# Kernel tuning notes

Hardware: AMD Instinct MI355X
Metric: run time of the kernel (lower is better)

The kernel has to match this reference:

```python
import jax, jax.numpy as jnp
import numpy as np


def setup_inputs() -> dict:
    key = jax.random.key(0)
    N, C, H, W, D = 4, 128, 48, 48, 48
    x = jax.random.normal(key, (N, C, H, W, D), dtype=jnp.float32)
    return {"x": x}


def reference(x) -> jnp.ndarray:
    # Channel self-attention over flattened spatial dims.
    N, C, H, W, D = x.shape
    q = x.reshape(N, C, -1)                      # [N, C, S]
    # energy[n, i, j] = <channel i, channel j>
    energy = jnp.einsum('ncs,nms->ncm', q, q)    # [N, C, C]
    # max-subtract trick (note: softmax of (max - energy), NOT energy - max)
    energy_new = jnp.max(energy, axis=-1, keepdims=True) - energy
    attention = jax.nn.softmax(energy_new, axis=-1)  # [N, C, C]
    out = jnp.einsum('ncm,nms->ncs', attention, q)   # [N, C, S]
    return out.reshape(N, C, H, W, D)
```

## Files before the change

kernel.cpp:

```cpp
#include <hip/hip_runtime.h>
#include <math.h>


static constexpr int CN = 128;
static constexpr int SN = 110592;
static constexpr int NB = 4;

static constexpr int GB = 64;
static constexpr int GSL = SN / GB;
static constexpr int GCH = GSL / 64;

static constexpr int PB = 432;
static constexpr int PCH = 4;

typedef float  f32x4  __attribute__((ext_vector_type(4)));
typedef short  bf16x8 __attribute__((ext_vector_type(8)));
typedef unsigned short u16x8 __attribute__((ext_vector_type(8)));
typedef unsigned short u16x4 __attribute__((ext_vector_type(4)));

__device__ __forceinline__ unsigned int splitpack(float v) {
    unsigned int u = __float_as_uint(v);
    unsigned int h = (u + 0x7fffu + ((u >> 16) & 1u)) >> 16;
    float lf = v - __uint_as_float(h << 16);
    unsigned int ul = __float_as_uint(lf);
    unsigned int l = (ul + 0x7fffu + ((ul >> 16) & 1u)) >> 16;
    return (l << 16) | (h & 0xffffu);
}
__device__ __forceinline__ unsigned short f2bh(float v) {
    unsigned int u = __float_as_uint(v);
    return (unsigned short)((u + 0x7fffu + ((u >> 16) & 1u)) >> 16);
}

__device__ __forceinline__ bf16x8 ldsfrag(const unsigned short* base, int row, int kbyte, int pitchB) {
    const char* p = reinterpret_cast<const char*>(base) + row * pitchB + (kbyte ^ ((row & 7) << 4));
    return *reinterpret_cast<const bf16x8*>(p);
}
__device__ __forceinline__ f32x4 mm(bf16x8 a, bf16x8 b, f32x4 c) {
    return __builtin_amdgcn_mfma_f32_16x16x32_bf16(a, b, c, 0, 0, 0);
}

template <bool ATOMIC>
__global__ __launch_bounds__(512, 2) void gram_mfma(const float* __restrict__ x,
                                                    float* __restrict__ dst) {
    __shared__ __align__(16) unsigned short lh[2][CN * 64];
    __shared__ __align__(16) unsigned short ll[2][CN * 64];
    const int bx = blockIdx.x, n = blockIdx.y;
    const int tid = threadIdx.x;
    const int lane = tid & 63;
    const int w = tid >> 6;
    const int wr = w >> 2, wc = w & 3;
    const int ra = lane & 15, kg = lane >> 4;

    const int c  = tid >> 2;
    const int ks = (tid & 3) << 4;
    const float* gq = x + (size_t)n * CN * SN + (size_t)c * SN + bx * GSL;

    f32x4 acc[4][2];
#pragma unroll
    for (int a = 0; a < 4; ++a)
#pragma unroll
        for (int b = 0; b < 2; ++b) acc[a][b] = (f32x4){0.f, 0.f, 0.f, 0.f};

    float4 st[4];
    auto load_chunk = [&](int t) {
        const float4* p = reinterpret_cast<const float4*>(gq + t * 64 + ks);
        st[0] = p[0]; st[1] = p[1]; st[2] = p[2]; st[3] = p[3];
    };

    auto stage = [&](int buf) {
        u16x8 ha, hb, la, lb;
        unsigned int p;
#define CV8(hv, lv, i, val) { p = splitpack(val); hv[i] = (unsigned short)(p & 0xffffu); lv[i] = (unsigned short)(p >> 16); }
        CV8(ha, la, 0, st[0].x) CV8(ha, la, 1, st[0].y) CV8(ha, la, 2, st[0].z) CV8(ha, la, 3, st[0].w)
        CV8(ha, la, 4, st[1].x) CV8(ha, la, 5, st[1].y) CV8(ha, la, 6, st[1].z) CV8(ha, la, 7, st[1].w)
        CV8(hb, lb, 0, st[2].x) CV8(hb, lb, 1, st[2].y) CV8(hb, lb, 2, st[2].z) CV8(hb, lb, 3, st[2].w)
        CV8(hb, lb, 4, st[3].x) CV8(hb, lb, 5, st[3].y) CV8(hb, lb, 6, st[3].z) CV8(hb, lb, 7, st[3].w)
#undef CV8
        char* ph = reinterpret_cast<char*>(lh[buf]) + c * 128;
        char* pl = reinterpret_cast<char*>(ll[buf]) + c * 128;
        const int sw = (c & 7) << 4;
        const int k2 = ks * 2;
        *reinterpret_cast<u16x8*>(ph + (k2 ^ sw))        = ha;
        *reinterpret_cast<u16x8*>(ph + ((k2 + 16) ^ sw)) = hb;
        *reinterpret_cast<u16x8*>(pl + (k2 ^ sw))        = la;
        *reinterpret_cast<u16x8*>(pl + ((k2 + 16) ^ sw)) = lb;
    };

    auto compute = [&](int buf) {
        const unsigned short* LH = lh[buf];
        const unsigned short* LL = ll[buf];
#pragma unroll
        for (int kk = 0; kk < 2; ++kk) {
            const int kb = kk * 64 + (kg << 4);
            bf16x8 ah[4], al[4], bh[2], bl[2];
#pragma unroll
            for (int it = 0; it < 4; ++it) {
                const int row = wr * 64 + it * 16 + ra;
                ah[it] = ldsfrag(LH, row, kb, 128);
                al[it] = ldsfrag(LL, row, kb, 128);
            }
#pragma unroll
            for (int jt = 0; jt < 2; ++jt) {
                const int row = wc * 32 + jt * 16 + ra;
                bh[jt] = ldsfrag(LH, row, kb, 128);
                bl[jt] = ldsfrag(LL, row, kb, 128);
            }
#pragma unroll
            for (int it = 0; it < 4; ++it)
#pragma unroll
                for (int jt = 0; jt < 2; ++jt) {
                    acc[it][jt] = mm(ah[it], bh[jt], acc[it][jt]);
                    acc[it][jt] = mm(ah[it], bl[jt], acc[it][jt]);
                    acc[it][jt] = mm(al[it], bh[jt], acc[it][jt]);
                }
        }
    };

    load_chunk(0);
    for (int t = 0; t < GCH; ++t) {
        stage(t & 1);
        if (t < GCH - 1) load_chunk(t + 1);
        __syncthreads();
        compute(t & 1);
    }

    const int q4 = kg << 2;
    if (!ATOMIC) {
        float* P = dst + (size_t)(n * GB + bx) * (CN * CN);
#pragma unroll
        for (int it = 0; it < 4; ++it)
#pragma unroll
            for (int jt = 0; jt < 2; ++jt)
#pragma unroll
                for (int q = 0; q < 4; ++q)
                    P[(wr * 64 + it * 16 + q4 + q) * CN + wc * 32 + jt * 16 + ra] = acc[it][jt][q];
    } else {
        float* E = dst + (size_t)n * CN * CN;
#pragma unroll
        for (int it = 0; it < 4; ++it)
#pragma unroll
            for (int jt = 0; jt < 2; ++jt)
#pragma unroll
                for (int q = 0; q < 4; ++q)
                    atomicAdd(&E[(wr * 64 + it * 16 + q4 + q) * CN + wc * 32 + jt * 16 + ra], acc[it][jt][q]);
    }
}

template <bool REDUCE>
__global__ void finish_kernel(const float* __restrict__ src,
                              unsigned short* __restrict__ att_h) {
    const int i = blockIdx.x, n = blockIdx.y, l = threadIdx.x;
    float e0, e1;
    if (REDUCE) {
        const float* p = src + (size_t)n * GB * (CN * CN) + i * CN;
        e0 = 0.f; e1 = 0.f;
#pragma unroll 8
        for (int k = 0; k < GB; ++k) {
            e0 += p[(size_t)k * (CN * CN) + l];
            e1 += p[(size_t)k * (CN * CN) + l + 64];
        }
    } else {
        const float* E = src + ((size_t)n * CN + i) * CN;
        e0 = E[l]; e1 = E[l + 64];
    }
    float m = fminf(e0, e1);
#pragma unroll
    for (int off = 32; off > 0; off >>= 1) m = fminf(m, __shfl_xor(m, off));
    const float p0 = expf(m - e0);
    const float p1 = expf(m - e1);
    float s = p0 + p1;
#pragma unroll
    for (int off = 32; off > 0; off >>= 1) s += __shfl_xor(s, off);
    const float inv = 1.f / s;
    const size_t o = ((size_t)n * CN + i) * CN;
    att_h[o + l]      = f2bh(p0 * inv);
    att_h[o + l + 64] = f2bh(p1 * inv);
}

__global__ __launch_bounds__(512, 4) void pv_mfma(const float* __restrict__ x,
                                                  const unsigned short* __restrict__ att_h,
                                                  float* __restrict__ out) {
    __shared__ __align__(16) unsigned short qh[2][64 * CN];
    const int bx = blockIdx.x, n = blockIdx.y;
    const int tid = threadIdx.x;
    const int lane = tid & 63;
    const int w = tid >> 6;
    const int ra = lane & 15, kg = lane >> 4;

    bf16x8 a_h[4];
    {
        const size_t rowoff = ((size_t)n * CN + w * 16 + ra) * CN + kg * 8;
        const unsigned short* Ah = att_h + rowoff;
#pragma unroll
        for (int kk = 0; kk < 4; ++kk)
            a_h[kk] = *reinterpret_cast<const bf16x8*>(Ah + kk * 32);
    }

    const int j0 = (tid >> 4) * 4;
    const int s0 = (tid & 15) * 4;
    const float* gx = x + (size_t)n * CN * SN;
    const int sbase = bx * (PCH * 64);

    f32x4 st[4];
    auto load_chunk = [&](int sb) {
#pragma unroll
        for (int r = 0; r < 4; ++r)
            st[r] = *reinterpret_cast<const f32x4*>(gx + (size_t)(j0 + r) * SN + sb + s0);
    };

    auto stage = [&](int buf) {
        char* base = reinterpret_cast<char*>(qh[buf]);
#pragma unroll
        for (int r = 0; r < 4; ++r) {
            u16x4 hv;
            hv[0] = f2bh(st[0][r]);
            hv[1] = f2bh(st[1][r]);
            hv[2] = f2bh(st[2][r]);
            hv[3] = f2bh(st[3][r]);
            const int s = s0 + r;
            const int off = s * 256 + ((j0 * 2) ^ ((s & 7) << 4));
            *reinterpret_cast<u16x4*>(base + off) = hv;
        }
    };

    auto compute = [&](int buf, int sb) {
        const unsigned short* Q = qh[buf];
#pragma unroll
        for (int stile = 0; stile < 4; ++stile) {
            f32x4 acc = (f32x4){0.f, 0.f, 0.f, 0.f};
            const int srow = stile * 16 + ra;
#pragma unroll
            for (int kk = 0; kk < 4; ++kk) {
                const int kb = kk * 64 + (kg << 4);
                bf16x8 bh = ldsfrag(Q, srow, kb, 256);
                acc = mm(a_h[kk], bh, acc);
            }
            float* o = out + ((size_t)n * CN + w * 16 + (kg << 2)) * SN + sb + stile * 16 + ra;
#pragma unroll
            for (int q = 0; q < 4; ++q)
                __builtin_nontemporal_store(acc[q], o + (size_t)q * SN);
        }
    };

    load_chunk(sbase);
    for (int t = 0; t < PCH; ++t) {
        stage(t & 1);
        if (t < PCH - 1) load_chunk(sbase + (t + 1) * 64);
        __syncthreads();
        compute(t & 1, sbase + t * 64);
    }
}

extern "C" void kernel_launch(void* const* d_in, const int* in_sizes, int n_in,
                              void* d_out, int out_size, void* d_ws, size_t ws_size,
                              hipStream_t stream) {
    (void)in_sizes; (void)n_in; (void)out_size;
    const float* x = (const float*)d_in[0];
    float* out = (float*)d_out;

    float* energy = (float*)d_ws;
    unsigned short* att_h = (unsigned short*)(energy + (size_t)NB * CN * CN);
    float* part = (float*)(att_h + (size_t)NB * CN * CN);
    const size_t need =
        (size_t)NB * CN * CN * sizeof(float) +
        (size_t)NB * CN * CN * sizeof(unsigned short) +
        (size_t)NB * GB * CN * CN * sizeof(float);

    if (ws_size >= need) {
        gram_mfma<false><<<dim3(GB, NB), 512, 0, stream>>>(x, part);
        finish_kernel<true><<<dim3(CN, NB), 64, 0, stream>>>(part, att_h);
    } else {
        hipMemsetAsync(energy, 0, (size_t)NB * CN * CN * sizeof(float), stream);
        gram_mfma<true><<<dim3(GB, NB), 512, 0, stream>>>(x, energy);
        finish_kernel<false><<<dim3(CN, NB), 64, 0, stream>>>(energy, att_h);
    }
    pv_mfma<<<dim3(PB, NB), 512, 0, stream>>>(x, att_h, out);
}
```

Before: 138.4 us.

## Emit bf16 copy of input in gram kernel and reuse it in PV

```diff
diff --git a/kernel.cpp b/kernel.cpp
--- a/kernel.cpp
+++ b/kernel.cpp
@@ -39,9 +39,10 @@
     return __builtin_amdgcn_mfma_f32_16x16x32_bf16(a, b, c, 0, 0, 0);
 }
 
-template <bool ATOMIC>
+template <bool ATOMIC, bool WRITEXH>
 __global__ __launch_bounds__(512, 2) void gram_mfma(const float* __restrict__ x,
-                                                    float* __restrict__ dst) {
+                                                    float* __restrict__ dst,
+                                                    unsigned short* __restrict__ xh) {
     __shared__ __align__(16) unsigned short lh[2][CN * 64];
     __shared__ __align__(16) unsigned short ll[2][CN * 64];
     const int bx = blockIdx.x, n = blockIdx.y;
@@ -54,6 +55,8 @@
     const int c  = tid >> 2;
     const int ks = (tid & 3) << 4;
     const float* gq = x + (size_t)n * CN * SN + (size_t)c * SN + bx * GSL;
+    unsigned short* gxh = WRITEXH
+        ? xh + (size_t)n * CN * SN + (size_t)c * SN + bx * GSL : nullptr;
 
     f32x4 acc[4][2];
 #pragma unroll
@@ -67,7 +70,7 @@
         st[0] = p[0]; st[1] = p[1]; st[2] = p[2]; st[3] = p[3];
     };
 
-    auto stage = [&](int buf) {
+    auto stage = [&](int buf, int t) {
         u16x8 ha, hb, la, lb;
         unsigned int p;
 #define CV8(hv, lv, i, val) { p = splitpack(val); hv[i] = (unsigned short)(p & 0xffffu); lv[i] = (unsigned short)(p >> 16); }
@@ -84,6 +87,11 @@
         *reinterpret_cast<u16x8*>(ph + ((k2 + 16) ^ sw)) = hb;
         *reinterpret_cast<u16x8*>(pl + (k2 ^ sw))        = la;
         *reinterpret_cast<u16x8*>(pl + ((k2 + 16) ^ sw)) = lb;
+        if (WRITEXH) {
+            unsigned short* q = gxh + t * 64 + ks;
+            *reinterpret_cast<u16x8*>(q)     = ha;
+            *reinterpret_cast<u16x8*>(q + 8) = hb;
+        }
     };
 
     auto compute = [&](int buf) {
@@ -118,7 +126,7 @@
 
     load_chunk(0);
     for (int t = 0; t < GCH; ++t) {
-        stage(t & 1);
+        stage(t & 1, t);
         if (t < GCH - 1) load_chunk(t + 1);
         __syncthreads();
         compute(t & 1);
@@ -133,7 +141,8 @@
             for (int jt = 0; jt < 2; ++jt)
 #pragma unroll
                 for (int q = 0; q < 4; ++q)
-                    P[(wr * 64 + it * 16 + q4 + q) * CN + wc * 32 + jt * 16 + ra] = acc[it][jt][q];
+                    __builtin_nontemporal_store(acc[it][jt][q],
+                        &P[(wr * 64 + it * 16 + q4 + q) * CN + wc * 32 + jt * 16 + ra]);
     } else {
         float* E = dst + (size_t)n * CN * CN;
 #pragma unroll
@@ -156,8 +165,8 @@
         e0 = 0.f; e1 = 0.f;
 #pragma unroll 8
         for (int k = 0; k < GB; ++k) {
-            e0 += p[(size_t)k * (CN * CN) + l];
-            e1 += p[(size_t)k * (CN * CN) + l + 64];
+            e0 += __builtin_nontemporal_load(&p[(size_t)k * (CN * CN) + l]);
+            e1 += __builtin_nontemporal_load(&p[(size_t)k * (CN * CN) + l + 64]);
         }
     } else {
         const float* E = src + ((size_t)n * CN + i) * CN;
@@ -177,7 +186,8 @@
     att_h[o + l + 64] = f2bh(p1 * inv);
 }
 
-__global__ __launch_bounds__(512, 4) void pv_mfma(const float* __restrict__ x,
+template <bool XH>
+__global__ __launch_bounds__(512, 4) void pv_mfma(const void* __restrict__ qsrc,
                                                   const unsigned short* __restrict__ att_h,
                                                   float* __restrict__ out) {
     __shared__ __align__(16) unsigned short qh[2][64 * CN];
@@ -198,14 +208,23 @@
 
     const int j0 = (tid >> 4) * 4;
     const int s0 = (tid & 15) * 4;
-    const float* gx = x + (size_t)n * CN * SN;
     const int sbase = bx * (PCH * 64);
 
-    f32x4 st[4];
+    const float* gx = XH ? nullptr
+        : reinterpret_cast<const float*>(qsrc) + (size_t)n * CN * SN;
+    const unsigned short* gxh = XH
+        ? reinterpret_cast<const unsigned short*>(qsrc) + (size_t)n * CN * SN : nullptr;
+
+    f32x4 stf[4];
+    u16x4 sth[4];
     auto load_chunk = [&](int sb) {
 #pragma unroll
-        for (int r = 0; r < 4; ++r)
-            st[r] = *reinterpret_cast<const f32x4*>(gx + (size_t)(j0 + r) * SN + sb + s0);
+        for (int r = 0; r < 4; ++r) {
+            if (XH)
+                sth[r] = *reinterpret_cast<const u16x4*>(gxh + (size_t)(j0 + r) * SN + sb + s0);
+            else
+                stf[r] = *reinterpret_cast<const f32x4*>(gx + (size_t)(j0 + r) * SN + sb + s0);
+        }
     };
 
     auto stage = [&](int buf) {
@@ -213,10 +232,13 @@
 #pragma unroll
         for (int r = 0; r < 4; ++r) {
             u16x4 hv;
-            hv[0] = f2bh(st[0][r]);
-            hv[1] = f2bh(st[1][r]);
-            hv[2] = f2bh(st[2][r]);
-            hv[3] = f2bh(st[3][r]);
+            if (XH) {
+                hv[0] = sth[0][r]; hv[1] = sth[1][r];
+                hv[2] = sth[2][r]; hv[3] = sth[3][r];
+            } else {
+                hv[0] = f2bh(stf[0][r]); hv[1] = f2bh(stf[1][r]);
+                hv[2] = f2bh(stf[2][r]); hv[3] = f2bh(stf[3][r]);
+            }
             const int s = s0 + r;
             const int off = s * 256 + ((j0 * 2) ^ ((s & 7) << 4));
             *reinterpret_cast<u16x4*>(base + off) = hv;
@@ -261,18 +283,26 @@
     float* energy = (float*)d_ws;
     unsigned short* att_h = (unsigned short*)(energy + (size_t)NB * CN * CN);
     float* part = (float*)(att_h + (size_t)NB * CN * CN);
-    const size_t need =
+    unsigned short* xh = (unsigned short*)(part + (size_t)NB * GB * CN * CN);
+
+    const size_t need_part =
         (size_t)NB * CN * CN * sizeof(float) +
         (size_t)NB * CN * CN * sizeof(unsigned short) +
         (size_t)NB * GB * CN * CN * sizeof(float);
-
-    if (ws_size >= need) {
-        gram_mfma<false><<<dim3(GB, NB), 512, 0, stream>>>(x, part);
+    const size_t need_xh = need_part + (size_t)NB * CN * SN * sizeof(unsigned short);
+
+    if (ws_size >= need_xh) {
+        gram_mfma<false, true><<<dim3(GB, NB), 512, 0, stream>>>(x, part, xh);
         finish_kernel<true><<<dim3(CN, NB), 64, 0, stream>>>(part, att_h);
+        pv_mfma<true><<<dim3(PB, NB), 512, 0, stream>>>(xh, att_h, out);
+    } else if (ws_size >= need_part) {
+        gram_mfma<false, false><<<dim3(GB, NB), 512, 0, stream>>>(x, part, nullptr);
+        finish_kernel<true><<<dim3(CN, NB), 64, 0, stream>>>(part, att_h);
+        pv_mfma<false><<<dim3(PB, NB), 512, 0, stream>>>(x, att_h, out);
     } else {
         hipMemsetAsync(energy, 0, (size_t)NB * CN * CN * sizeof(float), stream);
-        gram_mfma<true><<<dim3(GB, NB), 512, 0, stream>>>(x, energy);
+        gram_mfma<true, false><<<dim3(GB, NB), 512, 0, stream>>>(x, energy, nullptr);
         finish_kernel<false><<<dim3(CN, NB), 64, 0, stream>>>(energy, att_h);
-    }
-    pv_mfma<<<dim3(PB, NB), 512, 0, stream>>>(x, att_h, out);
-}
+        pv_mfma<false><<<dim3(PB, NB), 512, 0, stream>>>(x, att_h, out);
+    }
+}
```

Result: slower. 152.4 us (+10.1%).

## Split gram K-dim across wave halves with LDS reduction; parallelize partial-sum finish

Applied to the files above, without the earlier changes.

```diff
diff --git a/kernel.cpp b/kernel.cpp
--- a/kernel.cpp
+++ b/kernel.cpp
@@ -40,7 +40,7 @@
 }
 
 template <bool ATOMIC>
-__global__ __launch_bounds__(512, 2) void gram_mfma(const float* __restrict__ x,
+__global__ __launch_bounds__(512, 1) void gram_mfma(const float* __restrict__ x,
                                                     float* __restrict__ dst) {
     __shared__ __align__(16) unsigned short lh[2][CN * 64];
     __shared__ __align__(16) unsigned short ll[2][CN * 64];
@@ -48,18 +48,19 @@
     const int tid = threadIdx.x;
     const int lane = tid & 63;
     const int w = tid >> 6;
-    const int wr = w >> 2, wc = w & 3;
+    const int wr = (w >> 1) & 1, wc = w & 1;
+    const int kh = w >> 2;
     const int ra = lane & 15, kg = lane >> 4;
 
     const int c  = tid >> 2;
     const int ks = (tid & 3) << 4;
     const float* gq = x + (size_t)n * CN * SN + (size_t)c * SN + bx * GSL;
 
-    f32x4 acc[4][2];
+    f32x4 acc[4][4];
 #pragma unroll
     for (int a = 0; a < 4; ++a)
 #pragma unroll
-        for (int b = 0; b < 2; ++b) acc[a][b] = (f32x4){0.f, 0.f, 0.f, 0.f};
+        for (int b = 0; b < 4; ++b) acc[a][b] = (f32x4){0.f, 0.f, 0.f, 0.f};
 
     float4 st[4];
     auto load_chunk = [&](int t) {
@@ -89,31 +90,28 @@
     auto compute = [&](int buf) {
         const unsigned short* LH = lh[buf];
         const unsigned short* LL = ll[buf];
-#pragma unroll
-        for (int kk = 0; kk < 2; ++kk) {
-            const int kb = kk * 64 + (kg << 4);
-            bf16x8 ah[4], al[4], bh[2], bl[2];
-#pragma unroll
-            for (int it = 0; it < 4; ++it) {
-                const int row = wr * 64 + it * 16 + ra;
-                ah[it] = ldsfrag(LH, row, kb, 128);
-                al[it] = ldsfrag(LL, row, kb, 128);
+        const int kb = (kh << 6) + (kg << 4);
+        bf16x8 ah[4], al[4], bh[4], bl[4];
+#pragma unroll
+        for (int it = 0; it < 4; ++it) {
+            const int row = wr * 64 + it * 16 + ra;
+            ah[it] = ldsfrag(LH, row, kb, 128);
+            al[it] = ldsfrag(LL, row, kb, 128);
+        }
+#pragma unroll
+        for (int jt = 0; jt < 4; ++jt) {
+            const int row = wc * 64 + jt * 16 + ra;
+            bh[jt] = ldsfrag(LH, row, kb, 128);
+            bl[jt] = ldsfrag(LL, row, kb, 128);
+        }
+#pragma unroll
+        for (int it = 0; it < 4; ++it)
+#pragma unroll
+            for (int jt = 0; jt < 4; ++jt) {
+                acc[it][jt] = mm(ah[it], bh[jt], acc[it][jt]);
+                acc[it][jt] = mm(ah[it], bl[jt], acc[it][jt]);
+                acc[it][jt] = mm(al[it], bh[jt], acc[it][jt]);
             }
-#pragma unroll
-            for (int jt = 0; jt < 2; ++jt) {
-                const int row = wc * 32 + jt * 16 + ra;
-                bh[jt] = ldsfrag(LH, row, kb, 128);
-                bl[jt] = ldsfrag(LL, row, kb, 128);
-            }
-#pragma unroll
-            for (int it = 0; it < 4; ++it)
-#pragma unroll
-                for (int jt = 0; jt < 2; ++jt) {
-                    acc[it][jt] = mm(ah[it], bh[jt], acc[it][jt]);
-                    acc[it][jt] = mm(ah[it], bl[jt], acc[it][jt]);
-                    acc[it][jt] = mm(al[it], bh[jt], acc[it][jt]);
-                }
-        }
     };
 
     load_chunk(0);
@@ -124,44 +122,74 @@
         compute(t & 1);
     }
 
-    const int q4 = kg << 2;
-    if (!ATOMIC) {
-        float* P = dst + (size_t)(n * GB + bx) * (CN * CN);
+    __syncthreads();
+    float* ex = (w & 2) ? reinterpret_cast<float*>(ll[w & 1])
+                        : reinterpret_cast<float*>(lh[w & 1]);
+    if (w >= 4) {
 #pragma unroll
         for (int it = 0; it < 4; ++it)
 #pragma unroll
-            for (int jt = 0; jt < 2; ++jt)
-#pragma unroll
-                for (int q = 0; q < 4; ++q)
-                    P[(wr * 64 + it * 16 + q4 + q) * CN + wc * 32 + jt * 16 + ra] = acc[it][jt][q];
-    } else {
-        float* E = dst + (size_t)n * CN * CN;
+            for (int jt = 0; jt < 4; ++jt)
+                *reinterpret_cast<f32x4*>(ex + (it * 4 + jt) * 256 + lane * 4) = acc[it][jt];
+    }
+    __syncthreads();
+    if (w < 4) {
 #pragma unroll
         for (int it = 0; it < 4; ++it)
 #pragma unroll
-            for (int jt = 0; jt < 2; ++jt)
-#pragma unroll
-                for (int q = 0; q < 4; ++q)
-                    atomicAdd(&E[(wr * 64 + it * 16 + q4 + q) * CN + wc * 32 + jt * 16 + ra], acc[it][jt][q]);
+            for (int jt = 0; jt < 4; ++jt)
+                acc[it][jt] += *reinterpret_cast<const f32x4*>(ex + (it * 4 + jt) * 256 + lane * 4);
+
+        const int q4 = kg << 2;
+        if (!ATOMIC) {
+            float* P = dst + (size_t)(n * GB + bx) * (CN * CN);
+#pragma unroll
+            for (int it = 0; it < 4; ++it)
+#pragma unroll
+                for (int jt = 0; jt < 4; ++jt)
+#pragma unroll
+                    for (int q = 0; q < 4; ++q)
+                        __builtin_nontemporal_store(acc[it][jt][q],
+                            &P[(wr * 64 + it * 16 + q4 + q) * CN + wc * 64 + jt * 16 + ra]);
+        } else {
+            float* E = dst + (size_t)n * CN * CN;
+#pragma unroll
+            for (int it = 0; it < 4; ++it)
+#pragma unroll
+                for (int jt = 0; jt < 4; ++jt)
+#pragma unroll
+                    for (int q = 0; q < 4; ++q)
+                        atomicAdd(&E[(wr * 64 + it * 16 + q4 + q) * CN + wc * 64 + jt * 16 + ra], acc[it][jt][q]);
+        }
     }
 }
 
 template <bool REDUCE>
-__global__ void finish_kernel(const float* __restrict__ src,
-                              unsigned short* __restrict__ att_h) {
-    const int i = blockIdx.x, n = blockIdx.y, l = threadIdx.x;
-    float e0, e1;
+__global__ __launch_bounds__(256) void finish_kernel(const float* __restrict__ src,
+                                                     unsigned short* __restrict__ att_h) {
+    __shared__ float red[8][64];
+    const int i = blockIdx.x, n = blockIdx.y;
+    const int tid = threadIdx.x;
+    const int lane = tid & 63, w = tid >> 6;
+    float e0 = 0.f, e1 = 0.f;
     if (REDUCE) {
         const float* p = src + (size_t)n * GB * (CN * CN) + i * CN;
-        e0 = 0.f; e1 = 0.f;
-#pragma unroll 8
-        for (int k = 0; k < GB; ++k) {
-            e0 += p[(size_t)k * (CN * CN) + l];
-            e1 += p[(size_t)k * (CN * CN) + l + 64];
-        }
+#pragma unroll
+        for (int k = 0; k < GB / 4; ++k) {
+            const size_t o = (size_t)(w * (GB / 4) + k) * (CN * CN);
+            e0 += __builtin_nontemporal_load(&p[o + lane]);
+            e1 += __builtin_nontemporal_load(&p[o + lane + 64]);
+        }
+        red[w * 2][lane]     = e0;
+        red[w * 2 + 1][lane] = e1;
+        __syncthreads();
+        if (w != 0) return;
+        e0 = ((red[0][lane] + red[2][lane]) + (red[4][lane] + red[6][lane]));
+        e1 = ((red[1][lane] + red[3][lane]) + (red[5][lane] + red[7][lane]));
     } else {
+        if (w != 0) return;
         const float* E = src + ((size_t)n * CN + i) * CN;
-        e0 = E[l]; e1 = E[l + 64];
+        e0 = E[lane]; e1 = E[lane + 64];
     }
     float m = fminf(e0, e1);
 #pragma unroll
@@ -173,8 +201,8 @@
     for (int off = 32; off > 0; off >>= 1) s += __shfl_xor(s, off);
     const float inv = 1.f / s;
     const size_t o = ((size_t)n * CN + i) * CN;
-    att_h[o + l]      = f2bh(p0 * inv);
-    att_h[o + l + 64] = f2bh(p1 * inv);
+    att_h[o + lane]      = f2bh(p0 * inv);
+    att_h[o + lane + 64] = f2bh(p1 * inv);
 }
 
 __global__ __launch_bounds__(512, 4) void pv_mfma(const float* __restrict__ x,
@@ -268,11 +296,11 @@
 
     if (ws_size >= need) {
         gram_mfma<false><<<dim3(GB, NB), 512, 0, stream>>>(x, part);
-        finish_kernel<true><<<dim3(CN, NB), 64, 0, stream>>>(part, att_h);
+        finish_kernel<true><<<dim3(CN, NB), 256, 0, stream>>>(part, att_h);
     } else {
         hipMemsetAsync(energy, 0, (size_t)NB * CN * CN * sizeof(float), stream);
         gram_mfma<true><<<dim3(GB, NB), 512, 0, stream>>>(x, energy);
-        finish_kernel<false><<<dim3(CN, NB), 64, 0, stream>>>(energy, att_h);
+        finish_kernel<false><<<dim3(CN, NB), 256, 0, stream>>>(energy, att_h);
     }
     pv_mfma<<<dim3(PB, NB), 512, 0, stream>>>(x, att_h, out);
 }
```

After: 138.6 us. About the same (+0.2%).
